# Optimization experiments

Measured on AMD Instinct MI355X. Metric: run time of the kernel, lower is better.

## Reference

```python
import jax, jax.numpy as jnp
import numpy as np

C = 96        # channels
NH = 4        # num_heads
WIN = (2, 2, 2)
B, D, H, W = 2, 48, 48, 48
HID = 4 * C   # FFN hidden dim
EPS = 1e-5


def setup_inputs() -> dict:
    key = jax.random.key(0)
    ks = iter(jax.random.split(key, 64))
    def nrm(shape, scale=0.02):
        return jax.random.normal(next(ks), shape, jnp.float32) * scale
    inp = {
        "fg_feature": jax.random.normal(next(ks), (B, C, D, H, W), jnp.float32),
        "bg_feature": jax.random.normal(next(ks), (B, C, D, H, W), jnp.float32),
    }
    for p in ("fg", "bg"):
        inp[f"{p}_qn_w"] = jnp.ones((C,), jnp.float32)
        inp[f"{p}_qn_b"] = jnp.zeros((C,), jnp.float32)
        inp[f"{p}_kvn_w"] = jnp.ones((C,), jnp.float32)
        inp[f"{p}_kvn_b"] = jnp.zeros((C,), jnp.float32)
        inp[f"{p}_attn_in_w"] = nrm((3 * C, C))
        inp[f"{p}_attn_in_b"] = jnp.zeros((3 * C,), jnp.float32)
        inp[f"{p}_attn_out_w"] = nrm((C, C))
        inp[f"{p}_attn_out_b"] = jnp.zeros((C,), jnp.float32)
        inp[f"{p}_ffn_n_w"] = jnp.ones((C,), jnp.float32)
        inp[f"{p}_ffn_n_b"] = jnp.zeros((C,), jnp.float32)
        inp[f"{p}_ffn_w1"] = nrm((HID, C))
        inp[f"{p}_ffn_b1"] = jnp.zeros((HID,), jnp.float32)
        inp[f"{p}_ffn_w2"] = nrm((C, HID))
        inp[f"{p}_ffn_b2"] = jnp.zeros((C,), jnp.float32)
        inp[f"{p}_conv_w"] = nrm((C, C))  # 1x1x1 Conv3d kernel flattened to [Cout,Cin]
        inp[f"{p}_conv_b"] = jnp.zeros((C,), jnp.float32)
        inp[f"{p}_in_w"] = jnp.ones((C,), jnp.float32)
        inp[f"{p}_in_b"] = jnp.zeros((C,), jnp.float32)
    return inp


def _gelu(x):
    return jax.nn.gelu(x, approximate=False)  # torch nn.GELU default (erf)


def _ln(x, w, b):
    m = x.mean(-1, keepdims=True)
    v = ((x - m) ** 2).mean(-1, keepdims=True)
    return (x - m) * jax.lax.rsqrt(v + EPS) * w + b


def _window_partition(x):
    b, c, d, h, w = x.shape
    wd, wh, ww = WIN
    x = x.reshape(b, c, d // wd, wd, h // wh, wh, w // ww, ww)
    x = x.transpose(0, 2, 4, 6, 3, 5, 7, 1)
    return x.reshape(-1, wd * wh * ww, c)  # [num_windows, 8, C]


def _window_reverse(t, shape):
    b, c, d, h, w = shape
    wd, wh, ww = WIN
    x = t.reshape(b, d // wd, h // wh, w // ww, wd, wh, ww, c)
    x = x.transpose(0, 7, 1, 4, 2, 5, 3, 6)
    return x.reshape(b, c, d, h, w)


def _mha(q, k, v, Wi, bi, Wo, bo):
    # torch MultiheadAttention with packed in_proj, batch_first
    N, Lq, c = q.shape
    dh = c // NH
    qp = (q @ Wi[:c].T + bi[:c]).reshape(N, Lq, NH, dh)
    kp = (k @ Wi[c:2 * c].T + bi[c:2 * c]).reshape(N, -1, NH, dh)
    vp = (v @ Wi[2 * c:].T + bi[2 * c:]).reshape(N, -1, NH, dh)
    att = jnp.einsum('nqhd,nkhd->nhqk', qp, kp) * (1.0 / np.sqrt(dh))
    att = jax.nn.softmax(att, axis=-1)
    o = jnp.einsum('nhqk,nkhd->nqhd', att, vp).reshape(N, Lq, c)
    return o @ Wo.T + bo


def _ffn(x, w1, b1, w2, b2):
    return _gelu(x @ w1.T + b1) @ w2.T + b2


def _proj(x, cw, cb, iw, ib):
    # 1x1x1 Conv3d -> InstanceNorm3d(affine) -> GELU
    y = jnp.einsum('bcdhw,oc->bodhw', x, cw) + cb[None, :, None, None, None]
    m = y.mean((2, 3, 4), keepdims=True)
    v = ((y - m) ** 2).mean((2, 3, 4), keepdims=True)
    y = (y - m) * jax.lax.rsqrt(v + EPS)
    y = y * iw[None, :, None, None, None] + ib[None, :, None, None, None]
    return _gelu(y)


def _forward(fg_feature, bg_feature,
             fg_qn_w, fg_qn_b, fg_kvn_w, fg_kvn_b,
             fg_attn_in_w, fg_attn_in_b, fg_attn_out_w, fg_attn_out_b,
             fg_ffn_n_w, fg_ffn_n_b, fg_ffn_w1, fg_ffn_b1, fg_ffn_w2, fg_ffn_b2,
             fg_conv_w, fg_conv_b, fg_in_w, fg_in_b,
             bg_qn_w, bg_qn_b, bg_kvn_w, bg_kvn_b,
             bg_attn_in_w, bg_attn_in_b, bg_attn_out_w, bg_attn_out_b,
             bg_ffn_n_w, bg_ffn_n_b, bg_ffn_w1, bg_ffn_b1, bg_ffn_w2, bg_ffn_b2,
             bg_conv_w, bg_conv_b, bg_in_w, bg_in_b):
    meta = fg_feature.shape
    fg_t = _window_partition(fg_feature)
    bg_t = _window_partition(bg_feature)
    fg_q = _ln(fg_t, fg_qn_w, fg_qn_b)
    bg_q = _ln(bg_t, bg_qn_w, bg_qn_b)
    fg_c = _ln(fg_t, fg_kvn_w, fg_kvn_b)
    bg_c = _ln(bg_t, bg_kvn_w, bg_kvn_b)
    fg_t = fg_t + _mha(fg_q, bg_c, bg_c, fg_attn_in_w, fg_attn_in_b, fg_attn_out_w, fg_attn_out_b)
    bg_t = bg_t + _mha(bg_q, fg_c, fg_c, bg_attn_in_w, bg_attn_in_b, bg_attn_out_w, bg_attn_out_b)
    fg_t = fg_t + _ffn(_ln(fg_t, fg_ffn_n_w, fg_ffn_n_b), fg_ffn_w1, fg_ffn_b1, fg_ffn_w2, fg_ffn_b2)
    bg_t = bg_t + _ffn(_ln(bg_t, bg_ffn_n_w, bg_ffn_n_b), bg_ffn_w1, bg_ffn_b1, bg_ffn_w2, bg_ffn_b2)
    fg = _window_reverse(fg_t, meta)
    bg = _window_reverse(bg_t, meta)
    fg = _proj(fg, fg_conv_w, fg_conv_b, fg_in_w, fg_in_b)
    bg = _proj(bg, bg_conv_w, bg_conv_b, bg_in_w, bg_in_b)
    return fg, bg


def reference(fg_feature, bg_feature,
              fg_qn_w, fg_qn_b, fg_kvn_w, fg_kvn_b,
              fg_attn_in_w, fg_attn_in_b, fg_attn_out_w, fg_attn_out_b,
              fg_ffn_n_w, fg_ffn_n_b, fg_ffn_w1, fg_ffn_b1, fg_ffn_w2, fg_ffn_b2,
              fg_conv_w, fg_conv_b, fg_in_w, fg_in_b,
              bg_qn_w, bg_qn_b, bg_kvn_w, bg_kvn_b,
              bg_attn_in_w, bg_attn_in_b, bg_attn_out_w, bg_attn_out_b,
              bg_ffn_n_w, bg_ffn_n_b, bg_ffn_w1, bg_ffn_b1, bg_ffn_w2, bg_ffn_b2,
              bg_conv_w, bg_conv_b, bg_in_w, bg_in_b):
    return _forward(fg_feature, bg_feature,
                    fg_qn_w, fg_qn_b, fg_kvn_w, fg_kvn_b,
                    fg_attn_in_w, fg_attn_in_b, fg_attn_out_w, fg_attn_out_b,
                    fg_ffn_n_w, fg_ffn_n_b, fg_ffn_w1, fg_ffn_b1, fg_ffn_w2, fg_ffn_b2,
                    fg_conv_w, fg_conv_b, fg_in_w, fg_in_b,
                    bg_qn_w, bg_qn_b, bg_kvn_w, bg_kvn_b,
                    bg_attn_in_w, bg_attn_in_b, bg_attn_out_w, bg_attn_out_b,
                    bg_ffn_n_w, bg_ffn_n_b, bg_ffn_w1, bg_ffn_b1, bg_ffn_w2, bg_ffn_b2,
                    bg_conv_w, bg_conv_b, bg_in_w, bg_in_b)
```

## Files before the change

kernel.cpp:

```cpp
#include <hip/hip_runtime.h>
#include <hip/hip_bf16.h>


#define G_TOK 221184
#define TOK_PER_B 110592
#define STREAM_ELEMS 21233664

typedef __attribute__((ext_vector_type(8))) short short8;
typedef __attribute__((ext_vector_type(4))) float f32x4;
typedef unsigned short ushort_t;
typedef unsigned int uint_t;

#define MFMA16 __builtin_amdgcn_mfma_f32_16x16x32_bf16

__device__ __forceinline__ float gelu_erf(float x) {
    return 0.5f * x * (1.0f + erff(x * 0.70710678118654752f));
}
__device__ __forceinline__ float gelu_tanh(float x) {
    float u = x * (1.5957691216f + 0.0713548163f * x * x);
    return x / (1.0f + __expf(-u));
}
__device__ __forceinline__ ushort_t bfb(float f) {
    __hip_bfloat16 h = __float2bfloat16(f);
    return *reinterpret_cast<ushort_t*>(&h);
}
__device__ __forceinline__ void unpack8(uint4 v, float* o) {
    o[0] = __uint_as_float(v.x << 16); o[1] = __uint_as_float(v.x & 0xffff0000u);
    o[2] = __uint_as_float(v.y << 16); o[3] = __uint_as_float(v.y & 0xffff0000u);
    o[4] = __uint_as_float(v.z << 16); o[5] = __uint_as_float(v.z & 0xffff0000u);
    o[6] = __uint_as_float(v.w << 16); o[7] = __uint_as_float(v.w & 0xffff0000u);
}
__device__ __forceinline__ uint4 pack8(const float* f) {
    uint4 v;
    v.x = (uint_t)bfb(f[0]) | ((uint_t)bfb(f[1]) << 16);
    v.y = (uint_t)bfb(f[2]) | ((uint_t)bfb(f[3]) << 16);
    v.z = (uint_t)bfb(f[4]) | ((uint_t)bfb(f[5]) << 16);
    v.w = (uint_t)bfb(f[6]) | ((uint_t)bfb(f[7]) << 16);
    return v;
}
__device__ __forceinline__ uint2 pack4(const float* f) {
    uint2 v;
    v.x = (uint_t)bfb(f[0]) | ((uint_t)bfb(f[1]) << 16);
    v.y = (uint_t)bfb(f[2]) | ((uint_t)bfb(f[3]) << 16);
    return v;
}
__device__ __forceinline__ short8 pks8(const float* f) {
    short8 r;
    #pragma unroll
    for (int j = 0; j < 8; ++j) r[j] = (short)bfb(f[j]);
    return r;
}

__global__ __launch_bounds__(256) void k_fold(
    const float* __restrict__ Wi, const float* __restrict__ bi,
    const float* __restrict__ Wo, const float* __restrict__ bo,
    const float* __restrict__ W1, const float* __restrict__ b1,
    const float* __restrict__ W2, const float* __restrict__ b2,
    const float* __restrict__ Wc,
    const float* __restrict__ qnw, const float* __restrict__ qnb,
    const float* __restrict__ kvw, const float* __restrict__ kvb,
    const float* __restrict__ fnw, const float* __restrict__ fnb,
    ushort_t* __restrict__ w, float* __restrict__ bs)
{
// ... 68 lines not shown
{
    __shared__ float tile[192 * 97];
    int blk = blockIdx.x;
    const float* src; ushort_t* X;
    if (blk < 1152) { src = srcf; X = Xf; }
    else            { src = srcb; X = Xb; blk -= 1152; }
    int b = blk / 576, rem = blk % 576, dw = rem / 24, hw = rem % 24;
    int tid = threadIdx.x;
    for (int i = tid; i < 384 * 48; i += 256) {
        int r = i / 48, w = i % 48;
        int c = r >> 2, d_off = (r >> 1) & 1, h_off = r & 1;
        float v = src[((((long)b * 96 + c) * 48 + dw * 2 + d_off) * 48 + hw * 2 + h_off) * 48 + w];
        int t = (w >> 1) * 8 + d_off * 4 + h_off * 2 + (w & 1);
        tile[t * 97 + c] = v;
    }
    __syncthreads();
    long base = ((((long)b * 24 + dw) * 24 + hw) * 24) * 8;
    for (int i = tid; i < 192 * 12; i += 256) {
        int t = i / 12, c8 = i % 12;
        *(uint4*)&X[(base + t) * 96 + c8 * 8] = pack8(&tile[t * 97 + c8 * 8]);
    }
}

__device__ __forceinline__ void stageW(ushort_t* WB, const ushort_t* Wsrc, int tid) {
    const uint4* s = (const uint4*)Wsrc;
    uint4* d = (uint4*)WB;
    #pragma unroll
    for (int i = 0; i < 5; ++i) {
        int idx = tid + i * 256;
        if (idx < 1152) d[idx] = s[idx];
    }
}

__device__ __forceinline__ void gemmT_stage(
    const short8* xb2, const ushort_t* __restrict__ W,
    const float* __restrict__ bias, ushort_t* outs,
    int mbase, int l15, int kb)
{
    const int ln8 = (kb * 16 + l15) * 8;
    #pragma unroll
    for (int t = 0; t < 6; ++t) {
        float4 bv = *(const float4*)&bias[t * 16 + kb * 4];
        f32x4 A0 = {bv.x, bv.y, bv.z, bv.w};
        f32x4 A1 = {bv.x, bv.y, bv.z, bv.w};
        #pragma unroll
        for (int u = 0; u < 3; ++u) {
            short8 bw = *(const short8*)&W[(t * 3 + u) * 512 + ln8];
            A0 = MFMA16(bw, xb2[u],     A0, 0, 0, 0);
            A1 = MFMA16(bw, xb2[3 + u], A1, 0, 0, 0);
        }
        float f0[4], f1[4];
        #pragma unroll
        for (int i = 0; i < 4; ++i) { f0[i] = A0[i]; f1[i] = A1[i]; }
        *(uint2*)&outs[(mbase + l15) * 104 + t * 16 + kb * 4]      = pack4(f0);
        *(uint2*)&outs[(mbase + 16 + l15) * 104 + t * 16 + kb * 4] = pack4(f1);
    }
}

__global__ __launch_bounds__(256, 2) void k_attn(
    ushort_t* __restrict__ Xf, ushort_t* __restrict__ Xb,
    const ushort_t* __restrict__ wf, const ushort_t* __restrict__ wb,
    const float* __restrict__ bsf, const float* __restrict__ bsb)
{
    __shared__ ushort_t qs[128 * 104];
    __shared__ ushort_t kv[128 * 104];
    __shared__ ushort_t WB[9216];
    int tid = threadIdx.x, lane = tid & 63, wv = tid >> 6, mbase = wv * 32;
    int l15 = lane & 15, kb = lane >> 4;
    long g0 = (long)blockIdx.x * 128;

    short8 fr[2][6];
    #pragma unroll
    for (int s = 0; s < 2; ++s) {
        #pragma unroll
        for (int m = 0; m < 2; ++m) {
            const ushort_t* px = (s ? Xb : Xf) + (g0 + mbase + m * 16 + l15) * 96 + kb * 8;
            float f[24];
            unpack8(*(const uint4*)px, f);
            unpack8(*(const uint4*)(px + 32), f + 8);
            unpack8(*(const uint4*)(px + 64), f + 16);
            float s1 = 0.f, s2 = 0.f;
            #pragma unroll
            for (int j = 0; j < 24; ++j) { s1 += f[j]; s2 += f[j] * f[j]; }
            s1 += __shfl_xor(s1, 16); s1 += __shfl_xor(s1, 32);
            s2 += __shfl_xor(s2, 16); s2 += __shfl_xor(s2, 32);
            float mm = s1 * (1.f / 96.f);
            float rr = rsqrtf(s2 * (1.f / 96.f) - mm * mm + 1e-5f);
            #pragma unroll
            for (int j = 0; j < 24; ++j) f[j] = (f[j] - mm) * rr;
            fr[s][m * 3 + 0] = pks8(f);
            fr[s][m * 3 + 1] = pks8(f + 8);
            fr[s][m * 3 + 2] = pks8(f + 16);
        }
    }

    for (int dir = 0; dir < 2; ++dir) {
        const ushort_t* W = dir ? wb : wf;
        const float* bs = dir ? bsb : bsf;
        ushort_t* X = dir ? Xb : Xf;

        stageW(WB, W, tid);            __syncthreads();
        gemmT_stage(fr[dir], WB, bs, qs, mbase, l15, kb);
        __syncthreads();
        stageW(WB, W + 9216, tid);     __syncthreads();
        gemmT_stage(fr[dir ^ 1], WB, bs + 96, kv, mbase, l15, kb);

        float sc[2][8], inv[2];
        #pragma unroll
        for (int it = 0; it < 2; ++it) {
            int idx = lane + 64 * it;
            int win = (idx >> 5) & 3, hd = (idx >> 3) & 3, q8 = idx & 7;
            int tq = mbase + win * 8 + q8, ko = hd * 24;
            float qf[24];
            #pragma unroll
            for (int u = 0; u < 3; ++u)
                unpack8(*(const uint4*)&qs[tq * 104 + ko + u * 8], qf + u * 8);
            float mx = -1e30f;
            #pragma unroll
            for (int j = 0; j < 8; ++j) {
                float s = 0.f;
                #pragma unroll
                for (int u = 0; u < 3; ++u) {
                    float kf[8];
                    unpack8(*(const uint4*)&kv[(mbase + win * 8 + j) * 104 + ko + u * 8], kf);
                    #pragma unroll
                    for (int d = 0; d < 8; ++d) s += qf[u * 8 + d] * kf[d];
                }
                sc[it][j] = s; mx = fmaxf(mx, s);
            }
            float sum = 0.f;
            #pragma unroll
            for (int j = 0; j < 8; ++j) { sc[it][j] = __expf(sc[it][j] - mx); sum += sc[it][j]; }
            inv[it] = 1.f / sum;
        }
        __syncthreads();
        stageW(WB, W + 18432, tid);    __syncthreads();
        gemmT_stage(fr[dir ^ 1], WB, bs + 192, kv, mbase, l15, kb);

        #pragma unroll
        for (int it = 0; it < 2; ++it) {
            int idx = lane + 64 * it;
            int win = (idx >> 5) & 3, hd = (idx >> 3) & 3, q8 = idx & 7;
            int tq = mbase + win * 8 + q8, ko = hd * 24;
            #pragma unroll
            for (int u = 0; u < 3; ++u) {
                float of8[8];
                #pragma unroll
                for (int d = 0; d < 8; ++d) of8[d] = 0.f;
                #pragma unroll
                for (int j = 0; j < 8; ++j) {
                    float vf[8];
                    unpack8(*(const uint4*)&kv[(mbase + win * 8 + j) * 104 + ko + u * 8], vf);
                    #pragma unroll
                    for (int d = 0; d < 8; ++d) of8[d] += sc[it][j] * vf[d];
                }
                #pragma unroll
                for (int d = 0; d < 8; ++d) of8[d] *= inv[it];
                *(uint4*)&qs[tq * 104 + ko + u * 8] = pack8(of8);
            }
        }
        __syncthreads();
        stageW(WB, W + 27648, tid);    __syncthreads();
        {
            short8 o0[6];
            #pragma unroll
            for (int m = 0; m < 2; ++m)
                #pragma unroll
                for (int u = 0; u < 3; ++u)
                    o0[m * 3 + u] = *(const short8*)&qs[(mbase + m * 16 + l15) * 104 + u * 32 + kb * 8];
            gemmT_stage(o0, WB, bs + 288, qs, mbase, l15, kb);
        }
        #pragma unroll
        for (int u = 0; u < 6; ++u) {
            int idx = lane + 64 * u;
            int r2 = idx / 12, c8 = idx % 12;
            ushort_t* p = X + (g0 + mbase + r2) * 96 + c8 * 8;
            float xv[8], av[8], o[8];
            unpack8(*(const uint4*)p, xv);
            unpack8(*(const uint4*)&qs[(mbase + r2) * 104 + c8 * 8], av);
            #pragma unroll
            for (int j = 0; j < 8; ++j) o[j] = xv[j] + av[j];
            *(uint4*)p = pack8(o);
        }
        __syncthreads();
    }
}

__global__ __launch_bounds__(256, 2) void k_ffn(
    ushort_t* __restrict__ Xf, ushort_t* __restrict__ Xb,
    const ushort_t* __restrict__ wf, const ushort_t* __restrict__ wb,
    const float* __restrict__ bsf, const float* __restrict__ bsb)
{
    __shared__ ushort_t H[128 * 104];
    __shared__ ushort_t WB[18432];
    int blk = blockIdx.x, tid = threadIdx.x;
    ushort_t* X; const ushort_t* W; const float* bs;
    if (blk < 1728) { X = Xf; W = wf; bs = bsf; }
    else            { X = Xb; W = wb; bs = bsb; blk -= 1728; }
    long g0 = (long)blk * 128;
    int lane = tid & 63, wv = tid >> 6, mbase = wv * 32;
    int l15 = lane & 15, kb = lane >> 4;
    const int ln8 = lane * 8;

    short8 xb2[6];
    #pragma unroll
    for (int m = 0; m < 2; ++m) {
        const ushort_t* px = X + (g0 + mbase + m * 16 + l15) * 96 + kb * 8;
        float f[24];
        unpack8(*(const uint4*)px, f);
        unpack8(*(const uint4*)(px + 32), f + 8);
        unpack8(*(const uint4*)(px + 64), f + 16);
        float s1 = 0.f, s2 = 0.f;
        #pragma unroll
        for (int j = 0; j < 24; ++j) { s1 += f[j]; s2 += f[j] * f[j]; }
        s1 += __shfl_xor(s1, 16); s1 += __shfl_xor(s1, 32);
        s2 += __shfl_xor(s2, 16); s2 += __shfl_xor(s2, 32);
        float mm = s1 * (1.f / 96.f);
        float rr = rsqrtf(s2 * (1.f / 96.f) - mm * mm + 1e-5f);
        #pragma unroll
        for (int j = 0; j < 24; ++j) f[j] = (f[j] - mm) * rr;
        xb2[m * 3 + 0] = pks8(f); xb2[m * 3 + 1] = pks8(f + 8); xb2[m * 3 + 2] = pks8(f + 16);
    }

    const ushort_t* W1 = W + 36864;
    const ushort_t* W2 = W + 73728;
    const ushort_t* Wc = W + 110592;
    const float* b1 = bs + 384;
    const float* b2 = bs + 768;

    f32x4 acc2[2][6];
    #pragma unroll
    for (int t = 0; t < 6; ++t) {
        float4 bv = *(const float4*)&b2[t * 16 + kb * 4];
        acc2[0][t] = {bv.x, bv.y, bv.z, bv.w};
        acc2[1][t] = {bv.x, bv.y, bv.z, bv.w};
    }
    for (int ch = 0; ch < 4; ++ch) {
        {
            const uint4* s1 = (const uint4*)(W1 + ch * 9216);
            const uint4* s2 = (const uint4*)(W2 + ch * 9216);
            uint4* d = (uint4*)WB;
            #pragma unroll
            for (int i = 0; i < 5; ++i) {
                int idx = tid + i * 256;
                if (idx < 1152) { d[idx] = s1[idx]; d[1152 + idx] = s2[idx]; }
            }
        }
        __syncthreads();
        #pragma unroll
        for (int t = 0; t < 6; ++t) {
            float4 bv = *(const float4*)&b1[ch * 96 + t * 16 + kb * 4];
            f32x4 A0 = {bv.x, bv.y, bv.z, bv.w};
            f32x4 A1 = {bv.x, bv.y, bv.z, bv.w};
            #pragma unroll
            for (int u = 0; u < 3; ++u) {
                short8 bw = *(const short8*)&WB[(t * 3 + u) * 512 + ln8];
                A0 = MFMA16(bw, xb2[u],     A0, 0, 0, 0);
                A1 = MFMA16(bw, xb2[3 + u], A1, 0, 0, 0);
            }
            float q0[4], q1[4];
            #pragma unroll
            for (int i = 0; i < 4; ++i) { q0[i] = gelu_tanh(A0[i]); q1[i] = gelu_tanh(A1[i]); }
            *(uint2*)&H[(mbase + l15) * 104 + t * 16 + kb * 4]      = pack4(q0);
            *(uint2*)&H[(mbase + 16 + l15) * 104 + t * 16 + kb * 4] = pack4(q1);
        }
        short8 h0[3], h1[3];
        #pragma unroll
        for (int u = 0; u < 3; ++u) {
            h0[u] = *(const short8*)&H[(mbase + l15) * 104 + u * 32 + kb * 8];
            h1[u] = *(const short8*)&H[(mbase + 16 + l15) * 104 + u * 32 + kb * 8];
        }
        #pragma unroll
        for (int t = 0; t < 6; ++t) {
            #pragma unroll
            for (int u = 0; u < 3; ++u) {
                short8 bw = *(const short8*)&WB[9216 + (t * 3 + u) * 512 + ln8];
                acc2[0][t] = MFMA16(bw, h0[u], acc2[0][t], 0, 0, 0);
                acc2[1][t] = MFMA16(bw, h1[u], acc2[1][t], 0, 0, 0);
            }
        }
        __syncthreads();
    }
    {
        const uint4* sc_ = (const uint4*)Wc;
        uint4* d = (uint4*)WB;
        #pragma unroll
        for (int i = 0; i < 5; ++i) {
            int idx = tid + i * 256;
            if (idx < 1152) d[idx] = sc_[idx];
        }
    }
    #pragma unroll
    for (int t = 0; t < 6; ++t) {
        float f0[4], f1[4];
        #pragma unroll
        for (int i = 0; i < 4; ++i) { f0[i] = acc2[0][t][i]; f1[i] = acc2[1][t][i]; }
        *(uint2*)&H[(mbase + l15) * 104 + t * 16 + kb * 4]      = pack4(f0);
        *(uint2*)&H[(mbase + 16 + l15) * 104 + t * 16 + kb * 4] = pack4(f1);
    }
    #pragma unroll
    for (int u = 0; u < 6; ++u) {
        int idx = lane + 64 * u;
        int r2 = idx / 12, c8 = idx % 12;
        float xv[8], fv[8], y[8];
        unpack8(*(const uint4*)(X + (g0 + mbase + r2) * 96 + c8 * 8), xv);
        unpack8(*(const uint4*)&H[(mbase + r2) * 104 + c8 * 8], fv);
        #pragma unroll
        for (int j = 0; j < 8; ++j) y[j] = xv[j] + fv[j];
        *(uint4*)&H[(mbase + r2) * 104 + c8 * 8] = pack8(y);
    }
    __syncthreads();
    short8 y0[3], y1[3];
    #pragma unroll
    for (int u = 0; u < 3; ++u) {
        y0[u] = *(const short8*)&H[(mbase + l15) * 104 + u * 32 + kb * 8];
        y1[u] = *(const short8*)&H[(mbase + 16 + l15) * 104 + u * 32 + kb * 8];
    }
    #pragma unroll
    for (int t = 0; t < 6; ++t) {
        f32x4 A0 = {0.f, 0.f, 0.f, 0.f}, A1 = {0.f, 0.f, 0.f, 0.f};
        #pragma unroll
        for (int u = 0; u < 3; ++u) {
            short8 bw = *(const short8*)&WB[(t * 3 + u) * 512 + ln8];
            A0 = MFMA16(bw, y0[u], A0, 0, 0, 0);
            A1 = MFMA16(bw, y1[u], A1, 0, 0, 0);
        }
        float o0[4], o1[4];
        #pragma unroll
        for (int i = 0; i < 4; ++i) { o0[i] = A0[i]; o1[i] = A1[i]; }
        *(uint2*)&H[(mbase + l15) * 104 + t * 16 + kb * 4]      = pack4(o0);
        *(uint2*)&H[(mbase + 16 + l15) * 104 + t * 16 + kb * 4] = pack4(o1);
    }
    #pragma unroll
    for (int u = 0; u < 6; ++u) {
        int idx = lane + 64 * u;
        int r2 = idx / 12, c8 = idx % 12;
        *(uint4*)(X + (g0 + mbase + r2) * 96 + c8 * 8) =
            *(const uint4*)&H[(mbase + r2) * 104 + c8 * 8];
    }
}

__global__ __launch_bounds__(384) void k_instats(
    const ushort_t* __restrict__ Xf, const ushort_t* __restrict__ Xb,
    float* __restrict__ partial)
{
    __shared__ float red[2][32][96];
    int blk = blockIdx.x;
    const ushort_t* X = (blk < 108) ? Xf : Xb;
    int rem = blk % 108;
    int b = rem / 54, chunk = rem % 54;
    int tid = threadIdx.x;
    int c8 = tid % 12, slot = tid / 12;
    long base = (long)b * TOK_PER_B + chunk * 2048;
    float s8[8], ss8[8];
    #pragma unroll
    for (int j = 0; j < 8; ++j) { s8[j] = 0.f; ss8[j] = 0.f; }
    for (int i = 0; i < 64; ++i) {
        long row = base + i * 32 + slot;
        float f[8];
        unpack8(*(const uint4*)&X[row * 96 + c8 * 8], f);
        #pragma unroll
        for (int j = 0; j < 8; ++j) { s8[j] += f[j]; ss8[j] += f[j] * f[j]; }
    }
    #pragma unroll
    for (int j = 0; j < 8; ++j) {
        red[0][slot][c8 * 8 + j] = s8[j];
        red[1][slot][c8 * 8 + j] = ss8[j];
    }
    __syncthreads();
    if (tid < 96) {
        float S = 0.f, SS = 0.f;
        for (int sl = 0; sl < 32; ++sl) { S += red[0][sl][tid]; SS += red[1][sl][tid]; }
        partial[((long)blockIdx.x * 96 + tid) * 2]     = S;
        partial[((long)blockIdx.x * 96 + tid) * 2 + 1] = SS;
    }
}

__global__ __launch_bounds__(384) void k_infin(
    const float* __restrict__ partial, float* __restrict__ inMR)
{
    int tid = threadIdx.x;
    int s = tid / 192, rem = tid % 192, b = rem / 96, c = rem % 96;
    float S = 0.f, SS = 0.f;
    for (int ch = 0; ch < 54; ++ch) {
        int blk = s * 108 + b * 54 + ch;
        S  += partial[(blk * 96 + c) * 2];
        SS += partial[(blk * 96 + c) * 2 + 1];
    }
    float m = S * (1.f / 110592.f);
    float var = SS * (1.f / 110592.f) - m * m;
    inMR[tid * 2] = m;
    inMR[tid * 2 + 1] = rsqrtf(var + 1e-5f);
}

__global__ __launch_bounds__(256) void k_scatter(
    const ushort_t* __restrict__ Xf, const ushort_t* __restrict__ Xb,
    const float* __restrict__ inMR,
    const float* __restrict__ iwf, const float* __restrict__ ibf,
    const float* __restrict__ iwb, const float* __restrict__ ibb,
    float* __restrict__ out)
{
    __shared__ float tile[192 * 97];
    int blk = blockIdx.x, s = 0;
    const ushort_t* X = Xf; const float* iw = iwf; const float* ib = ibf;
    if (blk >= 1152) { s = 1; X = Xb; iw = iwb; ib = ibb; blk -= 1152; }
    int b = blk / 576, rem = blk % 576, dw = rem / 24, hw = rem % 24;
    int tid = threadIdx.x;
    long base = ((((long)b * 24 + dw) * 24 + hw) * 24) * 8;
    for (int i = tid; i < 192 * 12; i += 256) {
        int t = i / 12, c8 = i % 12;
        float f[8]; unpack8(*(const uint4*)&X[(base + t) * 96 + c8 * 8], f);
        #pragma unroll
        for (int j = 0; j < 8; ++j) tile[t * 97 + c8 * 8 + j] = f[j];
    }
    __syncthreads();
    float* o = out + (long)s * STREAM_ELEMS;
    for (int i = tid; i < 384 * 48; i += 256) {
        int r = i / 48, w = i % 48;
        int c = r >> 2, d_off = (r >> 1) & 1, h_off = r & 1;
        int t = (w >> 1) * 8 + d_off * 4 + h_off * 2 + (w & 1);
        float v = tile[t * 97 + c];
        float m  = inMR[((s * 2 + b) * 96 + c) * 2];
        float rr = inMR[((s * 2 + b) * 96 + c) * 2 + 1];
        v = (v - m) * rr * iw[c] + ib[c];
        o[((((long)b * 96 + c) * 48 + dw * 2 + d_off) * 48 + hw * 2 + h_off) * 48 + w] = gelu_erf(v);
    }
}

extern "C" void kernel_launch(void* const* d_in, const int* in_sizes, int n_in,
                              void* d_out, int out_size, void* d_ws, size_t ws_size,
                              hipStream_t stream)
{
    #define IN(i) ((const float*)d_in[i])
    ushort_t* Xf = (ushort_t*)d_ws;
    ushort_t* Xb = Xf + (long)STREAM_ELEMS;
    ushort_t* wW  = Xb + (long)STREAM_ELEMS;
    ushort_t* wWb = wW + 119808;
    float* bsf = (float*)(wWb + 119808);
    float* bsb = bsf + 864;
    float* partial = bsb + 864;
    float* inMR = partial + 41472;

    k_fold<<<128, 256, 0, stream>>>(IN(6), IN(7), IN(8), IN(9), IN(12), IN(13), IN(14), IN(15), IN(16),
                                    IN(2), IN(3), IN(22), IN(23), IN(10), IN(11), wW, bsf);
    k_fold<<<128, 256, 0, stream>>>(IN(24), IN(25), IN(26), IN(27), IN(30), IN(31), IN(32), IN(33), IN(34),
                                    IN(20), IN(21), IN(4), IN(5), IN(28), IN(29), wWb, bsb);

    k_gather<<<2304, 256, 0, stream>>>(IN(0), IN(1), Xf, Xb);

    k_attn<<<1728, 256, 0, stream>>>(Xf, Xb, wW, wWb, bsf, bsb);

    k_ffn<<<3456, 256, 0, stream>>>(Xf, Xb, wW, wWb, bsf, bsb);

    k_instats<<<216, 384, 0, stream>>>(Xf, Xb, partial);
    k_infin<<<1, 384, 0, stream>>>(partial, inMR);

    k_scatter<<<2304, 256, 0, stream>>>(Xf, Xb, inMR,
                                        IN(18), IN(19), IN(36), IN(37),
                                        (float*)d_out);
    #undef IN
}
```

Baseline: 637.0 us.

## Fuse attention, FFN, conv and instance-norm stats into one per-tile kernel

```diff
diff --git a/kernel.cpp b/kernel.cpp
--- a/kernel.cpp
+++ b/kernel.cpp
@@ -29,6 +29,9 @@
     o[2] = __uint_as_float(v.y << 16); o[3] = __uint_as_float(v.y & 0xffff0000u);
     o[4] = __uint_as_float(v.z << 16); o[5] = __uint_as_float(v.z & 0xffff0000u);
     o[6] = __uint_as_float(v.w << 16); o[7] = __uint_as_float(v.w & 0xffff0000u);
+}
+__device__ __forceinline__ void unpack8s(short8 v, float* o) {
+    unpack8(*(uint4*)&v, o);
 }
 __device__ __forceinline__ uint4 pack8(const float* f) {
     uint4 v;
@@ -188,28 +191,33 @@
     }
 }
 
-__global__ __launch_bounds__(256, 2) void k_attn(
+__global__ __launch_bounds__(256) void k_block(
     ushort_t* __restrict__ Xf, ushort_t* __restrict__ Xb,
     const ushort_t* __restrict__ wf, const ushort_t* __restrict__ wb,
-    const float* __restrict__ bsf, const float* __restrict__ bsb)
-{
-    __shared__ ushort_t qs[128 * 104];
-    __shared__ ushort_t kv[128 * 104];
-    __shared__ ushort_t WB[9216];
+    const float* __restrict__ bsf, const float* __restrict__ bsb,
+    float* __restrict__ partial)
+{
+    __shared__ __align__(16) ushort_t qs[128 * 104];
+    __shared__ __align__(16) ushort_t kv[128 * 104];
+    __shared__ __align__(16) ushort_t WB[9216];
     int tid = threadIdx.x, lane = tid & 63, wv = tid >> 6, mbase = wv * 32;
     int l15 = lane & 15, kb = lane >> 4;
     long g0 = (long)blockIdx.x * 128;
 
-    short8 fr[2][6];
+    short8 xraw[2][6], fr[2][6];
     #pragma unroll
     for (int s = 0; s < 2; ++s) {
         #pragma unroll
         for (int m = 0; m < 2; ++m) {
             const ushort_t* px = (s ? Xb : Xf) + (g0 + mbase + m * 16 + l15) * 96 + kb * 8;
+            uint4 v0 = *(const uint4*)px;
+            uint4 v1 = *(const uint4*)(px + 32);
+            uint4 v2 = *(const uint4*)(px + 64);
+            xraw[s][m * 3 + 0] = *(short8*)&v0;
+            xraw[s][m * 3 + 1] = *(short8*)&v1;
+            xraw[s][m * 3 + 2] = *(short8*)&v2;
             float f[24];
-            unpack8(*(const uint4*)px, f);
-            unpack8(*(const uint4*)(px + 32), f + 8);
-            unpack8(*(const uint4*)(px + 64), f + 16);
+            unpack8(v0, f); unpack8(v1, f + 8); unpack8(v2, f + 16);
             float s1 = 0.f, s2 = 0.f;
             #pragma unroll
             for (int j = 0; j < 24; ++j) { s1 += f[j]; s2 += f[j] * f[j]; }
@@ -225,10 +233,10 @@
         }
     }
 
+    #pragma unroll
     for (int dir = 0; dir < 2; ++dir) {
         const ushort_t* W = dir ? wb : wf;
         const float* bs = dir ? bsb : bsf;
-        ushort_t* X = dir ? Xb : Xf;
 
         stageW(WB, W, tid);            __syncthreads();
         gemmT_stage(fr[dir], WB, bs, qs, mbase, l15, kb);
@@ -302,226 +310,202 @@
             gemmT_stage(o0, WB, bs + 288, qs, mbase, l15, kb);
         }
         #pragma unroll
+        for (int m = 0; m < 2; ++m)
+            #pragma unroll
+            for (int u = 0; u < 3; ++u) {
+                short8 dD = *(const short8*)&qs[(mbase + m * 16 + l15) * 104 + u * 32 + kb * 8];
+                float xa[8], da[8];
+                unpack8s(xraw[dir][m * 3 + u], xa);
+                unpack8s(dD, da);
+                #pragma unroll
+                for (int j = 0; j < 8; ++j) xa[j] += da[j];
+                xraw[dir][m * 3 + u] = pks8(xa);
+            }
+        __syncthreads();
+    }
+
+    float* red = (float*)&kv[10240];
+    #pragma unroll
+    for (int s = 0; s < 2; ++s) {
+        const ushort_t* W = s ? wb : wf;
+        const float* bs = s ? bsb : bsf;
+        ushort_t* X = s ? Xb : Xf;
+        const ushort_t* W1 = W + 36864;
+        const ushort_t* W2 = W + 73728;
+        const ushort_t* Wc = W + 110592;
+        const float* b1 = bs + 384;
+        const float* b2 = bs + 768;
+        const int ln8 = lane * 8;
+
+        #pragma unroll
+        for (int m = 0; m < 2; ++m) {
+            float f[24];
+            unpack8s(xraw[s][m * 3 + 0], f);
+            unpack8s(xraw[s][m * 3 + 1], f + 8);
+            unpack8s(xraw[s][m * 3 + 2], f + 16);
+            float s1 = 0.f, s2 = 0.f;
+            #pragma unroll
+            for (int j = 0; j < 24; ++j) { s1 += f[j]; s2 += f[j] * f[j]; }
+            s1 += __shfl_xor(s1, 16); s1 += __shfl_xor(s1, 32);
+            s2 += __shfl_xor(s2, 16); s2 += __shfl_xor(s2, 32);
+            float mm = s1 * (1.f / 96.f);
+            float rr = rsqrtf(s2 * (1.f / 96.f) - mm * mm + 1e-5f);
+            #pragma unroll
+            for (int j = 0; j < 24; ++j) f[j] = (f[j] - mm) * rr;
+            fr[s][m * 3 + 0] = pks8(f);
+            fr[s][m * 3 + 1] = pks8(f + 8);
+            fr[s][m * 3 + 2] = pks8(f + 16);
+        }
+
+        f32x4 acc2[2][6];
+        #pragma unroll
+        for (int t = 0; t < 6; ++t) {
+            float4 bv = *(const float4*)&b2[t * 16 + kb * 4];
+            acc2[0][t] = {bv.x, bv.y, bv.z, bv.w};
+            acc2[1][t] = {bv.x, bv.y, bv.z, bv.w};
+        }
+        for (int ch = 0; ch < 4; ++ch) {
+            {
+                const uint4* s1p = (const uint4*)(W1 + ch * 9216);
+                const uint4* s2p = (const uint4*)(W2 + ch * 9216);
+                uint4* d1 = (uint4*)WB;
+                uint4* d2 = (uint4*)kv;
+                #pragma unroll
+                for (int i = 0; i < 5; ++i) {
+                    int idx = tid + i * 256;
+                    if (idx < 1152) { d1[idx] = s1p[idx]; d2[idx] = s2p[idx]; }
+                }
+            }
+            __syncthreads();
+            #pragma unroll
+            for (int t = 0; t < 6; ++t) {
+                float4 bv = *(const float4*)&b1[ch * 96 + t * 16 + kb * 4];
+                f32x4 A0 = {bv.x, bv.y, bv.z, bv.w};
+                f32x4 A1 = {bv.x, bv.y, bv.z, bv.w};
+                #pragma unroll
+                for (int u = 0; u < 3; ++u) {
+                    short8 bw = *(const short8*)&WB[(t * 3 + u) * 512 + ln8];
+                    A0 = MFMA16(bw, fr[s][u],     A0, 0, 0, 0);
+                    A1 = MFMA16(bw, fr[s][3 + u], A1, 0, 0, 0);
+                }
+                float q0[4], q1[4];
+                #pragma unroll
+                for (int i = 0; i < 4; ++i) { q0[i] = gelu_tanh(A0[i]); q1[i] = gelu_tanh(A1[i]); }
+                *(uint2*)&qs[(mbase + l15) * 104 + t * 16 + kb * 4]      = pack4(q0);
+                *(uint2*)&qs[(mbase + 16 + l15) * 104 + t * 16 + kb * 4] = pack4(q1);
+            }
+            short8 h0[3], h1[3];
+            #pragma unroll
+            for (int u = 0; u < 3; ++u) {
+                h0[u] = *(const short8*)&qs[(mbase + l15) * 104 + u * 32 + kb * 8];
+                h1[u] = *(const short8*)&qs[(mbase + 16 + l15) * 104 + u * 32 + kb * 8];
+            }
+            #pragma unroll
+            for (int t = 0; t < 6; ++t) {
+                #pragma unroll
+                for (int u = 0; u < 3; ++u) {
+                    short8 bw = *(const short8*)&kv[(t * 3 + u) * 512 + ln8];
+                    acc2[0][t] = MFMA16(bw, h0[u], acc2[0][t], 0, 0, 0);
+                    acc2[1][t] = MFMA16(bw, h1[u], acc2[1][t], 0, 0, 0);
+                }
+            }
+            __syncthreads();
+        }
+        #pragma unroll
+        for (int t = 0; t < 6; ++t) {
+            float f0[4], f1[4];
+            #pragma unroll
+            for (int i = 0; i < 4; ++i) { f0[i] = acc2[0][t][i]; f1[i] = acc2[1][t][i]; }
+            *(uint2*)&kv[(mbase + l15) * 104 + t * 16 + kb * 4]      = pack4(f0);
+            *(uint2*)&kv[(mbase + 16 + l15) * 104 + t * 16 + kb * 4] = pack4(f1);
+        }
+        stageW(WB, Wc, tid);
+        __syncthreads();
+        short8 yfr[6];
+        #pragma unroll
+        for (int m = 0; m < 2; ++m)
+            #pragma unroll
+            for (int u = 0; u < 3; ++u) {
+                short8 F8 = *(const short8*)&kv[(mbase + m * 16 + l15) * 104 + u * 32 + kb * 8];
+                float xa[8], fa[8];
+                unpack8s(xraw[s][m * 3 + u], xa);
+                unpack8s(F8, fa);
+                #pragma unroll
+                for (int j = 0; j < 8; ++j) xa[j] += fa[j];
+                yfr[m * 3 + u] = pks8(xa);
+            }
+        f32x4 sS[6], sQ[6];
+        #pragma unroll
+        for (int t = 0; t < 6; ++t) {
+            f32x4 A0 = {0.f, 0.f, 0.f, 0.f}, A1 = {0.f, 0.f, 0.f, 0.f};
+            #pragma unroll
+            for (int u = 0; u < 3; ++u) {
+                short8 bw = *(const short8*)&WB[(t * 3 + u) * 512 + ln8];
+                A0 = MFMA16(bw, yfr[u],     A0, 0, 0, 0);
+                A1 = MFMA16(bw, yfr[3 + u], A1, 0, 0, 0);
+            }
+            sS[t] = A0 + A1;
+            sQ[t] = A0 * A0 + A1 * A1;
+            float o0[4], o1[4];
+            #pragma unroll
+            for (int i = 0; i < 4; ++i) { o0[i] = A0[i]; o1[i] = A1[i]; }
+            *(uint2*)&qs[(mbase + l15) * 104 + t * 16 + kb * 4]      = pack4(o0);
+            *(uint2*)&qs[(mbase + 16 + l15) * 104 + t * 16 + kb * 4] = pack4(o1);
+        }
+        #pragma unroll
+        for (int mask = 1; mask < 16; mask <<= 1) {
+            #pragma unroll
+            for (int t = 0; t < 6; ++t) {
+                #pragma unroll
+                for (int i = 0; i < 4; ++i) {
+                    sS[t][i] += __shfl_xor(sS[t][i], mask);
+                    sQ[t][i] += __shfl_xor(sQ[t][i], mask);
+                }
+            }
+        }
+        if (l15 == 0) {
+            #pragma unroll
+            for (int t = 0; t < 6; ++t)
+                #pragma unroll
+                for (int i = 0; i < 4; ++i) {
+                    red[0 * 384 + wv * 96 + t * 16 + kb * 4 + i] = sS[t][i];
+                    red[1 * 384 + wv * 96 + t * 16 + kb * 4 + i] = sQ[t][i];
+                }
+        }
+        #pragma unroll
         for (int u = 0; u < 6; ++u) {
             int idx = lane + 64 * u;
             int r2 = idx / 12, c8 = idx % 12;
-            ushort_t* p = X + (g0 + mbase + r2) * 96 + c8 * 8;
-            float xv[8], av[8], o[8];
-            unpack8(*(const uint4*)p, xv);
-            unpack8(*(const uint4*)&qs[(mbase + r2) * 104 + c8 * 8], av);
-            #pragma unroll
-            for (int j = 0; j < 8; ++j) o[j] = xv[j] + av[j];
-            *(uint4*)p = pack8(o);
-        }
-        __syncthreads();
-    }
-}
-
-__global__ __launch_bounds__(256, 2) void k_ffn(
-    ushort_t* __restrict__ Xf, ushort_t* __restrict__ Xb,
-    const ushort_t* __restrict__ wf, const ushort_t* __restrict__ wb,
-    const float* __restrict__ bsf, const float* __restrict__ bsb)
-{
-    __shared__ ushort_t H[128 * 104];
-    __shared__ ushort_t WB[18432];
-    int blk = blockIdx.x, tid = threadIdx.x;
-    ushort_t* X; const ushort_t* W; const float* bs;
-    if (blk < 1728) { X = Xf; W = wf; bs = bsf; }
-    else            { X = Xb; W = wb; bs = bsb; blk -= 1728; }
-    long g0 = (long)blk * 128;
-    int lane = tid & 63, wv = tid >> 6, mbase = wv * 32;
-    int l15 = lane & 15, kb = lane >> 4;
-    const int ln8 = lane * 8;
-
-    short8 xb2[6];
-    #pragma unroll
-    for (int m = 0; m < 2; ++m) {
-        const ushort_t* px = X + (g0 + mbase + m * 16 + l15) * 96 + kb * 8;
-        float f[24];
-        unpack8(*(const uint4*)px, f);
-        unpack8(*(const uint4*)(px + 32), f + 8);
-        unpack8(*(const uint4*)(px + 64), f + 16);
-        float s1 = 0.f, s2 = 0.f;
-        #pragma unroll
-        for (int j = 0; j < 24; ++j) { s1 += f[j]; s2 += f[j] * f[j]; }
-        s1 += __shfl_xor(s1, 16); s1 += __shfl_xor(s1, 32);
-        s2 += __shfl_xor(s2, 16); s2 += __shfl_xor(s2, 32);
-        float mm = s1 * (1.f / 96.f);
-        float rr = rsqrtf(s2 * (1.f / 96.f) - mm * mm + 1e-5f);
-        #pragma unroll
-        for (int j = 0; j < 24; ++j) f[j] = (f[j] - mm) * rr;
-        xb2[m * 3 + 0] = pks8(f); xb2[m * 3 + 1] = pks8(f + 8); xb2[m * 3 + 2] = pks8(f + 16);
-    }
-
-    const ushort_t* W1 = W + 36864;
-    const ushort_t* W2 = W + 73728;
-    const ushort_t* Wc = W + 110592;
-    const float* b1 = bs + 384;
-    const float* b2 = bs + 768;
-
-    f32x4 acc2[2][6];
-    #pragma unroll
-    for (int t = 0; t < 6; ++t) {
-        float4 bv = *(const float4*)&b2[t * 16 + kb * 4];
-        acc2[0][t] = {bv.x, bv.y, bv.z, bv.w};
-        acc2[1][t] = {bv.x, bv.y, bv.z, bv.w};
-    }
-    for (int ch = 0; ch < 4; ++ch) {
-        {
-            const uint4* s1 = (const uint4*)(W1 + ch * 9216);
-            const uint4* s2 = (const uint4*)(W2 + ch * 9216);
-            uint4* d = (uint4*)WB;
-            #pragma unroll
-            for (int i = 0; i < 5; ++i) {
-                int idx = tid + i * 256;
-                if (idx < 1152) { d[idx] = s1[idx]; d[1152 + idx] = s2[idx]; }
-            }
-        }
-        __syncthreads();
-        #pragma unroll
-        for (int t = 0; t < 6; ++t) {
-            float4 bv = *(const float4*)&b1[ch * 96 + t * 16 + kb * 4];
-            f32x4 A0 = {bv.x, bv.y, bv.z, bv.w};
-            f32x4 A1 = {bv.x, bv.y, bv.z, bv.w};
-            #pragma unroll
-            for (int u = 0; u < 3; ++u) {
-                short8 bw = *(const short8*)&WB[(t * 3 + u) * 512 + ln8];
-                A0 = MFMA16(bw, xb2[u],     A0, 0, 0, 0);
-                A1 = MFMA16(bw, xb2[3 + u], A1, 0, 0, 0);
-            }
-            float q0[4], q1[4];
-            #pragma unroll
-            for (int i = 0; i < 4; ++i) { q0[i] = gelu_tanh(A0[i]); q1[i] = gelu_tanh(A1[i]); }
-            *(uint2*)&H[(mbase + l15) * 104 + t * 16 + kb * 4]      = pack4(q0);
-            *(uint2*)&H[(mbase + 16 + l15) * 104 + t * 16 + kb * 4] = pack4(q1);
-        }
-        short8 h0[3], h1[3];
-        #pragma unroll
-        for (int u = 0; u < 3; ++u) {
-            h0[u] = *(const short8*)&H[(mbase + l15) * 104 + u * 32 + kb * 8];
-            h1[u] = *(const short8*)&H[(mbase + 16 + l15) * 104 + u * 32 + kb * 8];
-        }
-        #pragma unroll
-        for (int t = 0; t < 6; ++t) {
-            #pragma unroll
-            for (int u = 0; u < 3; ++u) {
-                short8 bw = *(const short8*)&WB[9216 + (t * 3 + u) * 512 + ln8];
-                acc2[0][t] = MFMA16(bw, h0[u], acc2[0][t], 0, 0, 0);
-                acc2[1][t] = MFMA16(bw, h1[u], acc2[1][t], 0, 0, 0);
-            }
-        }
-        __syncthreads();
-    }
-    {
-        const uint4* sc_ = (const uint4*)Wc;
-        uint4* d = (uint4*)WB;
-        #pragma unroll
-        for (int i = 0; i < 5; ++i) {
-            int idx = tid + i * 256;
-            if (idx < 1152) d[idx] = sc_[idx];
-        }
-    }
-    #pragma unroll
-    for (int t = 0; t < 6; ++t) {
-        float f0[4], f1[4];
-        #pragma unroll
-        for (int i = 0; i < 4; ++i) { f0[i] = acc2[0][t][i]; f1[i] = acc2[1][t][i]; }
-        *(uint2*)&H[(mbase + l15) * 104 + t * 16 + kb * 4]      = pack4(f0);
-        *(uint2*)&H[(mbase + 16 + l15) * 104 + t * 16 + kb * 4] = pack4(f1);
-    }
-    #pragma unroll
-    for (int u = 0; u < 6; ++u) {
-        int idx = lane + 64 * u;
-        int r2 = idx / 12, c8 = idx % 12;
-        float xv[8], fv[8], y[8];
-        unpack8(*(const uint4*)(X + (g0 + mbase + r2) * 96 + c8 * 8), xv);
-        unpack8(*(const uint4*)&H[(mbase + r2) * 104 + c8 * 8], fv);
-        #pragma unroll
-        for (int j = 0; j < 8; ++j) y[j] = xv[j] + fv[j];
-        *(uint4*)&H[(mbase + r2) * 104 + c8 * 8] = pack8(y);
-    }
-    __syncthreads();
-    short8 y0[3], y1[3];
-    #pragma unroll
-    for (int u = 0; u < 3; ++u) {
-        y0[u] = *(const short8*)&H[(mbase + l15) * 104 + u * 32 + kb * 8];
-        y1[u] = *(const short8*)&H[(mbase + 16 + l15) * 104 + u * 32 + kb * 8];
-    }
-    #pragma unroll
-    for (int t = 0; t < 6; ++t) {
-        f32x4 A0 = {0.f, 0.f, 0.f, 0.f}, A1 = {0.f, 0.f, 0.f, 0.f};
-        #pragma unroll
-        for (int u = 0; u < 3; ++u) {
-            short8 bw = *(const short8*)&WB[(t * 3 + u) * 512 + ln8];
-            A0 = MFMA16(bw, y0[u], A0, 0, 0, 0);
-            A1 = MFMA16(bw, y1[u], A1, 0, 0, 0);
-        }
-        float o0[4], o1[4];
-        #pragma unroll
-        for (int i = 0; i < 4; ++i) { o0[i] = A0[i]; o1[i] = A1[i]; }
-        *(uint2*)&H[(mbase + l15) * 104 + t * 16 + kb * 4]      = pack4(o0);
-        *(uint2*)&H[(mbase + 16 + l15) * 104 + t * 16 + kb * 4] = pack4(o1);
-    }
-    #pragma unroll
-    for (int u = 0; u < 6; ++u) {
-        int idx = lane + 64 * u;
-        int r2 = idx / 12, c8 = idx % 12;
-        *(uint4*)(X + (g0 + mbase + r2) * 96 + c8 * 8) =
-            *(const uint4*)&H[(mbase + r2) * 104 + c8 * 8];
-    }
-}
-
-__global__ __launch_bounds__(384) void k_instats(
-    const ushort_t* __restrict__ Xf, const ushort_t* __restrict__ Xb,
-    float* __restrict__ partial)
-{
-    __shared__ float red[2][32][96];
-    int blk = blockIdx.x;
-    const ushort_t* X = (blk < 108) ? Xf : Xb;
-    int rem = blk % 108;
-    int b = rem / 54, chunk = rem % 54;
-    int tid = threadIdx.x;
-    int c8 = tid % 12, slot = tid / 12;
-    long base = (long)b * TOK_PER_B + chunk * 2048;
-    float s8[8], ss8[8];
-    #pragma unroll
-    for (int j = 0; j < 8; ++j) { s8[j] = 0.f; ss8[j] = 0.f; }
-    for (int i = 0; i < 64; ++i) {
-        long row = base + i * 32 + slot;
-        float f[8];
-        unpack8(*(const uint4*)&X[row * 96 + c8 * 8], f);
-        #pragma unroll
-        for (int j = 0; j < 8; ++j) { s8[j] += f[j]; ss8[j] += f[j] * f[j]; }
-    }
-    #pragma unroll
-    for (int j = 0; j < 8; ++j) {
-        red[0][slot][c8 * 8 + j] = s8[j];
-        red[1][slot][c8 * 8 + j] = ss8[j];
-    }
-    __syncthreads();
-    if (tid < 96) {
-        float S = 0.f, SS = 0.f;
-        for (int sl = 0; sl < 32; ++sl) { S += red[0][sl][tid]; SS += red[1][sl][tid]; }
-        partial[((long)blockIdx.x * 96 + tid) * 2]     = S;
-        partial[((long)blockIdx.x * 96 + tid) * 2 + 1] = SS;
-    }
-}
-
-__global__ __launch_bounds__(384) void k_infin(
+            *(uint4*)(X + (g0 + mbase + r2) * 96 + c8 * 8) =
+                *(const uint4*)&qs[(mbase + r2) * 104 + c8 * 8];
+        }
+        __syncthreads();
+        if (tid < 192) {
+            int which = tid / 96, c = tid % 96;
+            float v = red[which * 384 + c] + red[which * 384 + 96 + c]
+                    + red[which * 384 + 192 + c] + red[which * 384 + 288 + c];
+            partial[((long)blockIdx.x * 2 + s) * 192 + which * 96 + c] = v;
+        }
+        __syncthreads();
+    }
+}
+
+__global__ __launch_bounds__(96) void k_infin(
     const float* __restrict__ partial, float* __restrict__ inMR)
 {
-    int tid = threadIdx.x;
-    int s = tid / 192, rem = tid % 192, b = rem / 96, c = rem % 96;
+    int c = threadIdx.x;
+    int sb = blockIdx.x;
+    int s = sb >> 1, b = sb & 1;
     float S = 0.f, SS = 0.f;
-    for (int ch = 0; ch < 54; ++ch) {
-        int blk = s * 108 + b * 54 + ch;
-        S  += partial[(blk * 96 + c) * 2];
-        SS += partial[(blk * 96 + c) * 2 + 1];
+    for (int j = 0; j < 864; ++j) {
+        long base = ((long)(b * 864 + j) * 2 + s) * 192;
+        S  += partial[base + c];
+        SS += partial[base + 96 + c];
     }
     float m = S * (1.f / 110592.f);
     float var = SS * (1.f / 110592.f) - m * m;
-    inMR[tid * 2] = m;
-    inMR[tid * 2 + 1] = rsqrtf(var + 1e-5f);
+    inMR[(sb * 96 + c) * 2] = m;
+    inMR[(sb * 96 + c) * 2 + 1] = rsqrtf(var + 1e-5f);
 }
 
 __global__ __launch_bounds__(256) void k_scatter(
@@ -570,7 +554,7 @@
     float* bsf = (float*)(wWb + 119808);
     float* bsb = bsf + 864;
     float* partial = bsb + 864;
-    float* inMR = partial + 41472;
+    float* inMR = partial + 663552;
 
     k_fold<<<128, 256, 0, stream>>>(IN(6), IN(7), IN(8), IN(9), IN(12), IN(13), IN(14), IN(15), IN(16),
                                     IN(2), IN(3), IN(22), IN(23), IN(10), IN(11), wW, bsf);
@@ -579,12 +563,9 @@
 
     k_gather<<<2304, 256, 0, stream>>>(IN(0), IN(1), Xf, Xb);
 
-    k_attn<<<1728, 256, 0, stream>>>(Xf, Xb, wW, wWb, bsf, bsb);
-
-    k_ffn<<<3456, 256, 0, stream>>>(Xf, Xb, wW, wWb, bsf, bsb);
-
-    k_instats<<<216, 384, 0, stream>>>(Xf, Xb, partial);
-    k_infin<<<1, 384, 0, stream>>>(partial, inMR);
+    k_block<<<1728, 256, 0, stream>>>(Xf, Xb, wW, wWb, bsf, bsb, partial);
+
+    k_infin<<<4, 96, 0, stream>>>(partial, inMR);
 
     k_scatter<<<2304, 256, 0, stream>>>(Xf, Xb, inMR,
                                         IN(18), IN(19), IN(36), IN(37),
```

Result: slower. 835.2 us (+31.1%).

## Shrink attention tiles, read weights from global, and halve FFN weight LDS

Applied to the files above, without the earlier changes.

```diff
diff --git a/kernel.cpp b/kernel.cpp
--- a/kernel.cpp
+++ b/kernel.cpp
@@ -163,85 +163,73 @@
     }
 }
 
-__device__ __forceinline__ void gemmT_stage(
-    const short8* xb2, const ushort_t* __restrict__ W,
+__device__ __forceinline__ void gemmT16(
+    const short8* xb3, const ushort_t* __restrict__ W,
     const float* __restrict__ bias, ushort_t* outs,
-    int mbase, int l15, int kb)
-{
-    const int ln8 = (kb * 16 + l15) * 8;
+    int mbase, int l15, int kb, int ln8)
+{
     #pragma unroll
     for (int t = 0; t < 6; ++t) {
         float4 bv = *(const float4*)&bias[t * 16 + kb * 4];
         f32x4 A0 = {bv.x, bv.y, bv.z, bv.w};
-        f32x4 A1 = {bv.x, bv.y, bv.z, bv.w};
         #pragma unroll
         for (int u = 0; u < 3; ++u) {
             short8 bw = *(const short8*)&W[(t * 3 + u) * 512 + ln8];
-            A0 = MFMA16(bw, xb2[u],     A0, 0, 0, 0);
-            A1 = MFMA16(bw, xb2[3 + u], A1, 0, 0, 0);
-        }
-        float f0[4], f1[4];
-        #pragma unroll
-        for (int i = 0; i < 4; ++i) { f0[i] = A0[i]; f1[i] = A1[i]; }
-        *(uint2*)&outs[(mbase + l15) * 104 + t * 16 + kb * 4]      = pack4(f0);
-        *(uint2*)&outs[(mbase + 16 + l15) * 104 + t * 16 + kb * 4] = pack4(f1);
-    }
-}
-
-__global__ __launch_bounds__(256, 2) void k_attn(
+            A0 = MFMA16(bw, xb3[u], A0, 0, 0, 0);
+        }
+        float f0[4];
+        #pragma unroll
+        for (int i = 0; i < 4; ++i) f0[i] = A0[i];
+        *(uint2*)&outs[(mbase + l15) * 104 + t * 16 + kb * 4] = pack4(f0);
+    }
+}
+
+__global__ __launch_bounds__(256, 3) void k_attn(
     ushort_t* __restrict__ Xf, ushort_t* __restrict__ Xb,
     const ushort_t* __restrict__ wf, const ushort_t* __restrict__ wb,
     const float* __restrict__ bsf, const float* __restrict__ bsb)
 {
-    __shared__ ushort_t qs[128 * 104];
-    __shared__ ushort_t kv[128 * 104];
-    __shared__ ushort_t WB[9216];
-    int tid = threadIdx.x, lane = tid & 63, wv = tid >> 6, mbase = wv * 32;
+    __shared__ ushort_t qs[64 * 104];
+    __shared__ ushort_t kv[64 * 104];
+    int tid = threadIdx.x, lane = tid & 63, wv = tid >> 6, mbase = wv * 16;
     int l15 = lane & 15, kb = lane >> 4;
-    long g0 = (long)blockIdx.x * 128;
-
-    short8 fr[2][6];
+    const int ln8 = lane * 8;
+    long g0 = (long)blockIdx.x * 64;
+
+    short8 fr[2][3];
     #pragma unroll
     for (int s = 0; s < 2; ++s) {
-        #pragma unroll
-        for (int m = 0; m < 2; ++m) {
-            const ushort_t* px = (s ? Xb : Xf) + (g0 + mbase + m * 16 + l15) * 96 + kb * 8;
-            float f[24];
-            unpack8(*(const uint4*)px, f);
-            unpack8(*(const uint4*)(px + 32), f + 8);
-            unpack8(*(const uint4*)(px + 64), f + 16);
-            float s1 = 0.f, s2 = 0.f;
-            #pragma unroll
-            for (int j = 0; j < 24; ++j) { s1 += f[j]; s2 += f[j] * f[j]; }
-            s1 += __shfl_xor(s1, 16); s1 += __shfl_xor(s1, 32);
-            s2 += __shfl_xor(s2, 16); s2 += __shfl_xor(s2, 32);
-            float mm = s1 * (1.f / 96.f);
-            float rr = rsqrtf(s2 * (1.f / 96.f) - mm * mm + 1e-5f);
-            #pragma unroll
-            for (int j = 0; j < 24; ++j) f[j] = (f[j] - mm) * rr;
-            fr[s][m * 3 + 0] = pks8(f);
-            fr[s][m * 3 + 1] = pks8(f + 8);
-            fr[s][m * 3 + 2] = pks8(f + 16);
-        }
-    }
-
+        const ushort_t* px = (s ? Xb : Xf) + (g0 + mbase + l15) * 96 + kb * 8;
+        float f[24];
+        unpack8(*(const uint4*)px, f);
+        unpack8(*(const uint4*)(px + 32), f + 8);
+        unpack8(*(const uint4*)(px + 64), f + 16);
+        float s1 = 0.f, s2 = 0.f;
+        #pragma unroll
+        for (int j = 0; j < 24; ++j) { s1 += f[j]; s2 += f[j] * f[j]; }
+        s1 += __shfl_xor(s1, 16); s1 += __shfl_xor(s1, 32);
+        s2 += __shfl_xor(s2, 16); s2 += __shfl_xor(s2, 32);
+        float mm = s1 * (1.f / 96.f);
+        float rr = rsqrtf(s2 * (1.f / 96.f) - mm * mm + 1e-5f);
+        #pragma unroll
+        for (int j = 0; j < 24; ++j) f[j] = (f[j] - mm) * rr;
+        fr[s][0] = pks8(f); fr[s][1] = pks8(f + 8); fr[s][2] = pks8(f + 16);
+    }
+
+    int win = lane >> 5, hd = (lane >> 3) & 3, q8 = lane & 7;
+    int tq = mbase + win * 8 + q8, ko = hd * 24;
+
+    #pragma unroll
     for (int dir = 0; dir < 2; ++dir) {
         const ushort_t* W = dir ? wb : wf;
         const float* bs = dir ? bsb : bsf;
         ushort_t* X = dir ? Xb : Xf;
 
-        stageW(WB, W, tid);            __syncthreads();
-        gemmT_stage(fr[dir], WB, bs, qs, mbase, l15, kb);
-        __syncthreads();
-        stageW(WB, W + 9216, tid);     __syncthreads();
-        gemmT_stage(fr[dir ^ 1], WB, bs + 96, kv, mbase, l15, kb);
-
-        float sc[2][8], inv[2];
-        #pragma unroll
-        for (int it = 0; it < 2; ++it) {
-            int idx = lane + 64 * it;
-            int win = (idx >> 5) & 3, hd = (idx >> 3) & 3, q8 = idx & 7;
-            int tq = mbase + win * 8 + q8, ko = hd * 24;
+        gemmT16(fr[dir],     W,        bs,      qs, mbase, l15, kb, ln8);
+        gemmT16(fr[dir ^ 1], W + 9216, bs + 96, kv, mbase, l15, kb, ln8);
+
+        float sc[8], inv;
+        {
             float qf[24];
             #pragma unroll
             for (int u = 0; u < 3; ++u)
@@ -257,52 +245,42 @@
                     #pragma unroll
                     for (int d = 0; d < 8; ++d) s += qf[u * 8 + d] * kf[d];
                 }
-                sc[it][j] = s; mx = fmaxf(mx, s);
+                sc[j] = s; mx = fmaxf(mx, s);
             }
             float sum = 0.f;
             #pragma unroll
-            for (int j = 0; j < 8; ++j) { sc[it][j] = __expf(sc[it][j] - mx); sum += sc[it][j]; }
-            inv[it] = 1.f / sum;
-        }
-        __syncthreads();
-        stageW(WB, W + 18432, tid);    __syncthreads();
-        gemmT_stage(fr[dir ^ 1], WB, bs + 192, kv, mbase, l15, kb);
-
-        #pragma unroll
-        for (int it = 0; it < 2; ++it) {
-            int idx = lane + 64 * it;
-            int win = (idx >> 5) & 3, hd = (idx >> 3) & 3, q8 = idx & 7;
-            int tq = mbase + win * 8 + q8, ko = hd * 24;
-            #pragma unroll
-            for (int u = 0; u < 3; ++u) {
-                float of8[8];
+            for (int j = 0; j < 8; ++j) { sc[j] = __expf(sc[j] - mx); sum += sc[j]; }
+            inv = 1.f / sum;
+        }
+
+        gemmT16(fr[dir ^ 1], W + 18432, bs + 192, kv, mbase, l15, kb, ln8);
+
+        #pragma unroll
+        for (int u = 0; u < 3; ++u) {
+            float of8[8];
+            #pragma unroll
+            for (int d = 0; d < 8; ++d) of8[d] = 0.f;
+            #pragma unroll
+            for (int j = 0; j < 8; ++j) {
+                float vf[8];
+                unpack8(*(const uint4*)&kv[(mbase + win * 8 + j) * 104 + ko + u * 8], vf);
                 #pragma unroll
-                for (int d = 0; d < 8; ++d) of8[d] = 0.f;
-                #pragma unroll
-                for (int j = 0; j < 8; ++j) {
-                    float vf[8];
-                    unpack8(*(const uint4*)&kv[(mbase + win * 8 + j) * 104 + ko + u * 8], vf);
-                    #pragma unroll
-                    for (int d = 0; d < 8; ++d) of8[d] += sc[it][j] * vf[d];
-                }
-                #pragma unroll
-                for (int d = 0; d < 8; ++d) of8[d] *= inv[it];
-                *(uint4*)&qs[tq * 104 + ko + u * 8] = pack8(of8);
+                for (int d = 0; d < 8; ++d) of8[d] += sc[j] * vf[d];
             }
-        }
-        __syncthreads();
-        stageW(WB, W + 27648, tid);    __syncthreads();
+            #pragma unroll
+            for (int d = 0; d < 8; ++d) of8[d] *= inv;
+            *(uint4*)&qs[tq * 104 + ko + u * 8] = pack8(of8);
+        }
+
         {
-            short8 o0[6];
-            #pragma unroll
-            for (int m = 0; m < 2; ++m)
-                #pragma unroll
-                for (int u = 0; u < 3; ++u)
-                    o0[m * 3 + u] = *(const short8*)&qs[(mbase + m * 16 + l15) * 104 + u * 32 + kb * 8];
-            gemmT_stage(o0, WB, bs + 288, qs, mbase, l15, kb);
-        }
-        #pragma unroll
-        for (int u = 0; u < 6; ++u) {
+            short8 o0[3];
+            #pragma unroll
+            for (int u = 0; u < 3; ++u)
+                o0[u] = *(const short8*)&qs[(mbase + l15) * 104 + u * 32 + kb * 8];
+            gemmT16(o0, W + 27648, bs + 288, qs, mbase, l15, kb, ln8);
+        }
+        #pragma unroll
+        for (int u = 0; u < 3; ++u) {
             int idx = lane + 64 * u;
             int r2 = idx / 12, c8 = idx % 12;
             ushort_t* p = X + (g0 + mbase + r2) * 96 + c8 * 8;
@@ -313,17 +291,16 @@
             for (int j = 0; j < 8; ++j) o[j] = xv[j] + av[j];
             *(uint4*)p = pack8(o);
         }
-        __syncthreads();
-    }
-}
-
-__global__ __launch_bounds__(256, 2) void k_ffn(
+    }
+}
+
+__global__ __launch_bounds__(256, 3) void k_ffn(
     ushort_t* __restrict__ Xf, ushort_t* __restrict__ Xb,
     const ushort_t* __restrict__ wf, const ushort_t* __restrict__ wb,
     const float* __restrict__ bsf, const float* __restrict__ bsb)
 {
     __shared__ ushort_t H[128 * 104];
-    __shared__ ushort_t WB[18432];
+    __shared__ ushort_t WB[9216];
     int blk = blockIdx.x, tid = threadIdx.x;
     ushort_t* X; const ushort_t* W; const float* bs;
     if (blk < 1728) { X = Xf; W = wf; bs = bsf; }
@@ -367,16 +344,7 @@
         acc2[1][t] = {bv.x, bv.y, bv.z, bv.w};
     }
     for (int ch = 0; ch < 4; ++ch) {
-        {
-            const uint4* s1 = (const uint4*)(W1 + ch * 9216);
-            const uint4* s2 = (const uint4*)(W2 + ch * 9216);
-            uint4* d = (uint4*)WB;
-            #pragma unroll
-            for (int i = 0; i < 5; ++i) {
-                int idx = tid + i * 256;
-                if (idx < 1152) { d[idx] = s1[idx]; d[1152 + idx] = s2[idx]; }
-            }
-        }
+        stageW(WB, W1 + ch * 9216, tid);
         __syncthreads();
         #pragma unroll
         for (int t = 0; t < 6; ++t) {
@@ -395,6 +363,9 @@
             *(uint2*)&H[(mbase + l15) * 104 + t * 16 + kb * 4]      = pack4(q0);
             *(uint2*)&H[(mbase + 16 + l15) * 104 + t * 16 + kb * 4] = pack4(q1);
         }
+        __syncthreads();
+        stageW(WB, W2 + ch * 9216, tid);
+        __syncthreads();
         short8 h0[3], h1[3];
         #pragma unroll
         for (int u = 0; u < 3; ++u) {
@@ -405,22 +376,14 @@
         for (int t = 0; t < 6; ++t) {
             #pragma unroll
             for (int u = 0; u < 3; ++u) {
-                short8 bw = *(const short8*)&WB[9216 + (t * 3 + u) * 512 + ln8];
+                short8 bw = *(const short8*)&WB[(t * 3 + u) * 512 + ln8];
                 acc2[0][t] = MFMA16(bw, h0[u], acc2[0][t], 0, 0, 0);
                 acc2[1][t] = MFMA16(bw, h1[u], acc2[1][t], 0, 0, 0);
             }
         }
         __syncthreads();
     }
-    {
-        const uint4* sc_ = (const uint4*)Wc;
-        uint4* d = (uint4*)WB;
-        #pragma unroll
-        for (int i = 0; i < 5; ++i) {
-            int idx = tid + i * 256;
-            if (idx < 1152) d[idx] = sc_[idx];
-        }
-    }
+    stageW(WB, Wc, tid);
     #pragma unroll
     for (int t = 0; t < 6; ++t) {
         float f0[4], f1[4];
@@ -579,7 +542,7 @@
 
     k_gather<<<2304, 256, 0, stream>>>(IN(0), IN(1), Xf, Xb);
 
-    k_attn<<<1728, 256, 0, stream>>>(Xf, Xb, wW, wWb, bsf, bsb);
+    k_attn<<<3456, 256, 0, stream>>>(Xf, Xb, wW, wWb, bsf, bsb);
 
     k_ffn<<<3456, 256, 0, stream>>>(Xf, Xb, wW, wWb, bsf, bsb);
 
```

Result: faster. 619.9 us (-2.7%).
